# Optimization experiments

Hardware: AMD Instinct MI355X
Metric: run time of the kernel (lower is better)

The kernel has to match this reference:

```python
import jax, jax.numpy as jnp
import numpy as np

B, T, D, H, L, FF, V = 32, 64, 512, 8, 4, 2048, 128
HD = D // H
TEMP = 0.1
SCALE_BASE = 16.0
NEG = -1e9


def setup_inputs() -> dict:
    key = jax.random.key(0)
    cnt = [0]
    def nk():
        cnt[0] += 1
        return jax.random.fold_in(key, cnt[0])
    def rn(shape, s=0.02):
        return jax.random.normal(nk(), shape, dtype=jnp.float32) * s
    inp = {
        "target_tensor": jax.random.randint(nk(), (B, T), 0, V),
        "mol_encoding": jax.random.normal(nk(), (B, D), dtype=jnp.float32),
        "emb": rn((V, D), 1.0),
        "sa_in_w": rn((L, 3 * D, D)), "sa_in_b": jnp.zeros((L, 3 * D), jnp.float32),
        "sa_out_w": rn((L, D, D)), "sa_out_b": jnp.zeros((L, D), jnp.float32),
        "ca_in_w": rn((L, 3 * D, D)), "ca_in_b": jnp.zeros((L, 3 * D), jnp.float32),
        "ca_out_w": rn((L, D, D)), "ca_out_b": jnp.zeros((L, D), jnp.float32),
        "ff_w1": rn((L, FF, D)), "ff_b1": jnp.zeros((L, FF), jnp.float32),
        "ff_w2": rn((L, D, FF)), "ff_b2": jnp.zeros((L, D), jnp.float32),
        "n1_g": jnp.ones((L, D), jnp.float32), "n1_b": jnp.zeros((L, D), jnp.float32),
        "n2_g": jnp.ones((L, D), jnp.float32), "n2_b": jnp.zeros((L, D), jnp.float32),
        "n3_g": jnp.ones((L, D), jnp.float32), "n3_b": jnp.zeros((L, D), jnp.float32),
        "fn_g": jnp.ones((D,), jnp.float32), "fn_b": jnp.zeros((D,), jnp.float32),
        "out_w1": rn((2 * D, D)), "out_b1": jnp.zeros((2 * D,), jnp.float32),
        "out_w2": rn((1024, 2 * D)), "out_b2": jnp.zeros((1024,), jnp.float32),
        "out_w3": rn((V, 1024)), "out_b3": jnp.zeros((V,), jnp.float32),
    }
    return inp


def _ln(x, g, b, eps=1e-5):
    mu = x.mean(-1, keepdims=True)
    var = ((x - mu) ** 2).mean(-1, keepdims=True)
    return (x - mu) * jax.lax.rsqrt(var + eps) * g + b


def _xpos(x):
    # x: [B, T, D]; XPOS rotary with scale_base=16, downscale=False
    t, d = x.shape[1], x.shape[2]
    half = d // 2
    sv = (jnp.arange(0, d, 2, dtype=jnp.float32) + 0.4 * d) / (1.4 * d)      # [half]
    pos = jnp.arange(t, dtype=jnp.float32)
    scale = sv[None, :] ** (pos / SCALE_BASE)[:, None]                       # [t, half]
    inv_freq = 1.0 / (10000.0 ** (jnp.arange(half, dtype=jnp.float32) / half))
    ang = pos[:, None] * inv_freq[None, :]                                   # [t, half]
    sin = jnp.repeat(jnp.sin(ang) * scale, 2, axis=-1)                       # duplicate_interleave
    cos = jnp.repeat(jnp.cos(ang) * scale, 2, axis=-1)
    x1, x2 = x[..., ::2], x[..., 1::2]
    rot = jnp.stack((-x2, x1), axis=-1).reshape(x.shape)                     # rotate_every_two
    return x * cos + rot * sin


def _mha(q_in, k_in, v_in, in_w, in_b, out_w, out_b, mask):
    wq, wk, wv = jnp.split(in_w, 3, axis=0)
    bq, bk, bv = jnp.split(in_b, 3, axis=0)
    Bq, Tq = q_in.shape[0], q_in.shape[1]
    q = (q_in @ wq.T + bq).reshape(Bq, Tq, H, HD)
    k = (k_in @ wk.T + bk).reshape(Bq, -1, H, HD)
    v = (v_in @ wv.T + bv).reshape(Bq, -1, H, HD)
    scores = jnp.einsum('bqhd,bkhd->bhqk', q, k) / np.float32(np.sqrt(HD))
    if mask is not None:
        scores = jnp.where(mask, NEG, scores)
    p = jax.nn.softmax(scores, axis=-1)
    o = jnp.einsum('bhqk,bkhd->bqhd', p, v).reshape(Bq, Tq, D)
    return o @ out_w.T + out_b


def reference(target_tensor, mol_encoding, emb, sa_in_w, sa_in_b, sa_out_w, sa_out_b,
              ca_in_w, ca_in_b, ca_out_w, ca_out_b, ff_w1, ff_b1, ff_w2, ff_b2,
              n1_g, n1_b, n2_g, n2_b, n3_g, n3_b, fn_g, fn_b,
              out_w1, out_b1, out_w2, out_b2, out_w3, out_b3):
    memory = mol_encoding[:, None, :]                      # [B, 1, D]
    causal = jnp.triu(jnp.ones((T, T), bool), 1)
    samp_key = jax.random.key(1)

    def logits_at(pred, t):
        x = _xpos(emb[pred])                               # [B, T, D]
        mask = causal[None, None] | (pred == 0)[:, None, None, :]
        for i in range(L):
            a = _mha(x, x, x, sa_in_w[i], sa_in_b[i], sa_out_w[i], sa_out_b[i], mask)
            x = _ln(x + a, n1_g[i], n1_b[i])
            c = _mha(x, memory, memory, ca_in_w[i], ca_in_b[i], ca_out_w[i], ca_out_b[i], None)
            x = _ln(x + c, n2_g[i], n2_b[i])
            f = jax.nn.silu(x @ ff_w1[i].T + ff_b1[i]) @ ff_w2[i].T + ff_b2[i]
            x = _ln(x + f, n3_g[i], n3_b[i])
        x = _ln(x, fn_g, fn_b)
        h = jnp.take(x, t - 1, axis=1)                     # [B, D]
        h = jax.nn.gelu(h @ out_w1.T + out_b1, approximate=False)
        h = jax.nn.gelu(h @ out_w2.T + out_b2, approximate=False)
        return h @ out_w3.T + out_b3                       # [B, V]

    def step(pred, t):
        logits = logits_at(pred, t)
        lp = jax.nn.log_softmax(logits / TEMP, axis=-1)
        u = jax.random.uniform(jax.random.fold_in(samp_key, t), lp.shape)
        g = -jnp.log(-jnp.log(u + 1e-9) + 1e-9)
        tok = jnp.argmax(lp + g, axis=-1).astype(jnp.int32)
        return pred.at[:, t].set(tok), logits

    pred0 = jnp.zeros((B, T), jnp.int32).at[:, 0].set(1)
    pred, _ = jax.lax.scan(jax.checkpoint(step), pred0, jnp.arange(1, T))
    return pred
```

## Files before the change

kernel.cpp:

```cpp
#include <hip/hip_runtime.h>
#include <stdint.h>
#include <stddef.h>

#define BB 32
#define TT 64
#define DD 512
#define HH 8
#define HDIM 64
#define LL 4
#define FFD 2048
#define VV 128

#define NBLK 256
#define NTHR 512

__host__ __device__ inline uint32_t rotl32(uint32_t v, int n){ return (v << n) | (v >> (32 - n)); }

__host__ __device__ inline void tf2x32(uint32_t k0, uint32_t k1, uint32_t x0, uint32_t x1,
                                       uint32_t* o0, uint32_t* o1){
  uint32_t ks2 = k0 ^ k1 ^ 0x1BD11BDAu;
  x0 += k0; x1 += k1;
  x0 += x1; x1 = rotl32(x1,13); x1 ^= x0;
  x0 += x1; x1 = rotl32(x1,15); x1 ^= x0;
  x0 += x1; x1 = rotl32(x1,26); x1 ^= x0;
  x0 += x1; x1 = rotl32(x1, 6); x1 ^= x0;
  x0 += k1; x1 += ks2 + 1u;
  x0 += x1; x1 = rotl32(x1,17); x1 ^= x0;
  x0 += x1; x1 = rotl32(x1,29); x1 ^= x0;
  x0 += x1; x1 = rotl32(x1,16); x1 ^= x0;
  x0 += x1; x1 = rotl32(x1,24); x1 ^= x0;
  x0 += ks2; x1 += k0 + 2u;
  x0 += x1; x1 = rotl32(x1,13); x1 ^= x0;
  x0 += x1; x1 = rotl32(x1,15); x1 ^= x0;
  x0 += x1; x1 = rotl32(x1,26); x1 ^= x0;
  x0 += x1; x1 = rotl32(x1, 6); x1 ^= x0;
  x0 += k0; x1 += k1 + 3u;
  x0 += x1; x1 = rotl32(x1,17); x1 ^= x0;
  x0 += x1; x1 = rotl32(x1,29); x1 ^= x0;
  x0 += x1; x1 = rotl32(x1,16); x1 ^= x0;
  x0 += x1; x1 = rotl32(x1,24); x1 ^= x0;
  x0 += k1; x1 += ks2 + 4u;
  x0 += x1; x1 = rotl32(x1,13); x1 ^= x0;
  x0 += x1; x1 = rotl32(x1,15); x1 ^= x0;
  x0 += x1; x1 = rotl32(x1,26); x1 ^= x0;
  x0 += x1; x1 = rotl32(x1, 6); x1 ^= x0;
  x0 += ks2; x1 += k0 + 5u;
  *o0 = x0; *o1 = x1;
}

__device__ inline float dot_f4(const float* __restrict__ a, const float* __restrict__ w, int K){
  float acc = 0.f;
  const float4* a4 = (const float4*)a;
  const float4* w4 = (const float4*)w;
  int K4 = K >> 2;
  for (int k = 0; k < K4; ++k){
    float4 av = a4[k], wv = w4[k];
    acc = fmaf(av.x, wv.x, acc);
    acc = fmaf(av.y, wv.y, acc);
    acc = fmaf(av.z, wv.z, acc);
    acc = fmaf(av.w, wv.w, acc);
  }
  return acc;
}

__device__ inline float block_ln(float v, float g, float bb, float* red){
  __syncthreads();
  float s = v;
  #pragma unroll
  for (int off = 32; off; off >>= 1) s += __shfl_xor(s, off);
  if ((threadIdx.x & 63) == 0) red[threadIdx.x >> 6] = s;
  __syncthreads();
  float mu = (red[0]+red[1]+red[2]+red[3]+red[4]+red[5]+red[6]+red[7]) * (1.0f/512.0f);
  float dv = v - mu;
  float sq = dv * dv;
  #pragma unroll
  for (int off = 32; off; off >>= 1) sq += __shfl_xor(sq, off);
  __syncthreads();
  if ((threadIdx.x & 63) == 0) red[threadIdx.x >> 6] = sq;
  __syncthreads();
  float var = (red[0]+red[1]+red[2]+red[3]+red[4]+red[5]+red[6]+red[7]) * (1.0f/512.0f);
  return dv * (1.0f / sqrtf(var + 1e-5f)) * g + bb;
}

__device__ inline float row_reduce(float v, int wid, int j, float* wred){
  #pragma unroll
  for (int off = 32; off; off >>= 1) v += __shfl_xor(v, off);
  if ((threadIdx.x & 63) == 0) wred[wid] = v;
  __syncthreads();
  float r = wred[2*j] + wred[2*j+1];
  __syncthreads();
  return r;
}

__device__ __forceinline__ void gbar(unsigned* bar, int g, int m, unsigned epoch){
  __syncthreads();
  if (threadIdx.x == 0){
    __builtin_amdgcn_fence(__ATOMIC_RELEASE, "agent");
    const int h   = m & 1;
    const int k   = m >> 1;
    const int sub = k >> 3;
    const int gh  = g*2 + h;
    unsigned* subcnt  = bar + gh*64 + sub*16;
    unsigned* halfcnt = bar + 1024 + gh*16;
    unsigned* hflag   = bar + 1280 + gh*16;
    unsigned* peer    = bar + 1280 + (g*2 + (1-h))*16;
    unsigned* hgen    = bar + 1536 + gh*16;
    unsigned old = __hip_atomic_fetch_add(subcnt, 1u, __ATOMIC_RELAXED, __HIP_MEMORY_SCOPE_AGENT);
    if (old == 8u*epoch - 1u){
      unsigned o2 = __hip_atomic_fetch_add(halfcnt, 1u, __ATOMIC_RELAXED, __HIP_MEMORY_SCOPE_AGENT);
      if (o2 == 4u*epoch - 1u){
        __hip_atomic_store(hflag, epoch, __ATOMIC_RELAXED, __HIP_MEMORY_SCOPE_AGENT);
        while (__hip_atomic_load(peer, __ATOMIC_RELAXED, __HIP_MEMORY_SCOPE_AGENT) < epoch)
          __builtin_amdgcn_s_sleep(1);
        __hip_atomic_store(hgen, epoch, __ATOMIC_RELAXED, __HIP_MEMORY_SCOPE_AGENT);
      }
    }
    while (__hip_atomic_load(hgen, __ATOMIC_RELAXED, __HIP_MEMORY_SCOPE_AGENT) < epoch)
      __builtin_amdgcn_s_sleep(1);
    __builtin_amdgcn_fence(__ATOMIC_ACQUIRE, "agent");
  }
  __syncthreads();
}

__global__ void k_tables(float* __restrict__ cosb, float* __restrict__ sinb){
  int tid = blockIdx.x * blockDim.x + threadIdx.x;
  int p = tid >> 8, i = tid & 255;
  float sv = (2.0f * (float)i + 204.8f) / 716.8f;
  float scale = powf(sv, (float)p / 16.0f);
  float invf = 1.0f / powf(10000.0f, (float)i / 256.0f);
  float ang = (float)p * invf;
  cosb[tid] = cosf(ang) * scale;
  sinb[tid] = sinf(ang) * scale;
}

__global__ void k_ca1(const float* __restrict__ mol, const float* __restrict__ w,
                      const float* __restrict__ bias, float* __restrict__ tmp){
  int tid = blockIdx.x * blockDim.x + threadIdx.x;
  int l = tid >> 14; int r = tid & 16383; int b = r >> 9; int d = r & 511;
  const float* wr = w + (size_t)l*3*DD*DD + (size_t)(2*DD + d)*DD;
  tmp[tid] = bias[l*3*DD + 2*DD + d] + dot_f4(mol + (size_t)b*DD, wr, DD);
}

__global__ void k_ca2(const float* __restrict__ tmp, const float* __restrict__ w,
                      const float* __restrict__ bias, float* __restrict__ cac){
  int tid = blockIdx.x * blockDim.x + threadIdx.x;
  int l = tid >> 14; int r = tid & 16383; int b = r >> 9; int d = r & 511;
  const float* wr = w + (size_t)l*DD*DD + (size_t)d*DD;
  cac[tid] = bias[l*DD + d] + dot_f4(tmp + ((size_t)l*BB + b)*DD, wr, DD);
}

__global__ void k_binit(unsigned* __restrict__ bar, int* __restrict__ pred){
  int tid = threadIdx.x;
  bar[tid] = 0u;
  bar[tid + 1024] = 0u;
  pred[tid]        = ((tid & (TT-1)) == 0) ? 1 : 0;
  pred[tid + 1024] = (((tid + 1024) & (TT-1)) == 0) ? 1 : 0;
}

__global__ void k_pack32(const float* __restrict__ in, float* __restrict__ out,
                         int N, int K, int total){
  int tid = blockIdx.x * blockDim.x + threadIdx.x;
  if (tid >= total) return;
  int S = N * K;
  int l = tid / S, r = tid - l*S;
  int k32 = r / (32*N);
  int r2 = r - k32*32*N;
  int n = r2 >> 5, ku = r2 & 31;
  out[tid] = in[(size_t)l*S + (size_t)n*K + k32*32 + ku];
}

#define CELL8(WARR, KOFF)                                                     \
  _Pragma("unroll")                                                           \
  for (int q = 0; q < 8; ++q){                                                \
    float4 w = WARR[q];                                                       \
    const int kk = (KOFF) + q*4;                                              \
    _Pragma("unroll")                                                         \
    for (int r_ = 0; r_ < 8; ++r_){                                           \
      float4 x = *(const float4*)&sxp[r_*512 + kk];                           \
      a[r_]=fmaf(w.x,x.x,a[r_]); a[r_]=fmaf(w.y,x.y,a[r_]);                   \
      a[r_]=fmaf(w.z,x.z,a[r_]); a[r_]=fmaf(w.w,x.w,a[r_]);                   \
    }                                                                         \
  }

struct KParams {
  const float *emb, *sab, *sob, *f1b, *f2b;
  const float *g1,*b1,*g2,*b2,*g3,*b3,*fg,*fb;
  const float *o1b,*o2b,*o3w,*o3b;
  const float *cosb,*sinb,*cac;
  const float *sawP,*sowP,*f1wP,*f2wP,*o1wP,*o2wP;
  float *kc,*vc,*xl,*qb,*at,*ao,*x2,*fo,*h1,*xf,*hh1,*hh2,*ps3;
  int *pred;
  unsigned *bar;
};

__global__ __launch_bounds__(NTHR) void k_persist(KParams P){
  const int bid = blockIdx.x, tid = threadIdx.x;
  const int g = bid & 3;
  const int m = bid >> 2;
  const int wid = tid >> 6, lane = tid & 63;
  __shared__ __align__(16) float smem[17472];
  unsigned epoch = 0;

  for (int t = 1; t < TT; ++t){
    const int pp = t - 1;

    for (int l = 0; l < LL; ++l){
      if (m < 24){
        float* sx   = smem;
        float* part = smem + 4096;
        float* srow = smem + 8192;
        if (l == 0){
          #pragma unroll
          for (int it = 0; it < 2; ++it){
            int j = it*4 + (tid >> 7), d4 = (tid & 127) * 4;
            int rb = g*8 + j;
            int tok = P.pred[rb*TT + pp];
            #pragma unroll
            for (int e = d4; e < d4 + 4; e += 2){
              int i = e >> 1;
              float c = P.cosb[pp*256 + i], s = P.sinb[pp*256 + i];
              float e0 = P.emb[(size_t)tok*DD + e];
              float e1 = P.emb[(size_t)tok*DD + e + 1];
              sx[j*512 + e]     = fmaf(e0, c, -(e1*s));
              sx[j*512 + e + 1] = fmaf(e1, c, e0*s);
            }
          }
        } else {
          if (tid < 8){
            float aa = 0.f, bq = 0.f;
            const float* pr = P.ps3 + (size_t)(g*8 + tid)*64;
            for (int s = 0; s < 32; ++s){ aa += pr[s*2]; bq += pr[s*2+1]; }
            float mu = aa * (1.0f/512.0f);
            float var = bq * (1.0f/512.0f) - mu*mu;
            srow[tid*2]   = mu;
            srow[tid*2+1] = 1.0f / sqrtf(var + 1e-5f);
          }
          __syncthreads();
          #pragma unroll
          for (int it = 0; it < 2; ++it){
            int j = it*4 + (tid >> 7), d4 = (tid & 127) * 4;
            int rb = g*8 + j;
            float mu = srow[j*2], rs = srow[j*2+1];
            float4 xv = *(const float4*)&P.x2[(size_t)rb*DD + d4];
            float4 fv = *(const float4*)&P.fo[(size_t)rb*DD + d4];
            const float* g3r = P.g3 + (size_t)(l-1)*DD;
            const float* b3r = P.b3 + (size_t)(l-1)*DD;
            float yv[4] = {xv.x+fv.x, xv.y+fv.y, xv.z+fv.z, xv.w+fv.w};
            #pragma unroll
            for (int i = 0; i < 4; ++i)
              sx[j*512 + d4 + i] = (yv[i]-mu)*rs*g3r[d4+i] + b3r[d4+i];
          }
        }
        __syncthreads();
        if (m == 0){
          #pragma unroll
          for (int it = 0; it < 2; ++it){
            int j = it*4 + (tid >> 7), d4 = (tid & 127) * 4;
            *(float4*)&P.xl[(size_t)(g*8+j)*DD + d4] = *(float4*)&sx[j*512 + d4];
          }
        }
        const int n0 = m*64;
        const float4* wb0 = (const float4*)P.sawP + ((size_t)l*16 + wid*2)*(1536*8)
                          + (size_t)(n0 + lane)*8;
        const float4* wb1 = wb0 + 1536*8;
        float4 w0[8], w1[8];
        #pragma unroll
        for (int q = 0; q < 8; ++q) w0[q] = wb0[q];
        #pragma unroll
        for (int q = 0; q < 8; ++q) w1[q] = wb1[q];
        float a[8] = {0.f,0.f,0.f,0.f,0.f,0.f,0.f,0.f};
        const float* sxp = sx;
        const int kb = wid*64;
        CELL8(w0, kb);
        CELL8(w1, kb + 32);
        #pragma unroll
        for (int r_ = 0; r_ < 8; ++r_) part[(wid*8 + r_)*64 + lane] = a[r_];
        __syncthreads();
        {
          int jr = tid >> 6, nl = tid & 63;
          int n = n0 + nl, rb2 = g*8 + jr;
          float s = P.sab[l*1536 + n];
          #pragma unroll
          for (int w = 0; w < 8; ++w) s += part[(w*8+jr)*64 + nl];
          if (n < DD){
            P.qb[(size_t)rb2*DD + n] = s;
          } else if (n < 2*DD){
            int h = (n - DD) >> 6, hd = (n - DD) & 63;
            P.kc[((((size_t)l*BB + rb2)*HH + h)*TT + pp)*HDIM + hd] = s;
          } else {
            int h = (n - 2*DD) >> 6, hd = (n - 2*DD) & 63;
            P.vc[((((size_t)l*BB + rb2)*HH + h)*TT + pp)*HDIM + hd] = s;
          }
        }
      }
      gbar(P.bar, g, m, ++epoch);

      {
        int bl = m >> 3, h = m & 7, rb = g*8 + bl;
        float* qs = smem; float* ps = smem + 64;
        if (tid < 64) qs[tid] = P.qb[(size_t)rb*DD + h*HDIM + tid];
        __syncthreads();
        if (tid < 64){
          const float* kb = P.kc + (((size_t)l*BB + rb)*HH + h)*TT*HDIM;
          float s = -INFINITY;
          if (lane <= pp && P.pred[rb*TT + lane] != 0){
            const float* kr = kb + lane*HDIM;
            float acc = 0.f;
            #pragma unroll
            for (int k2 = 0; k2 < HDIM; ++k2) acc = fmaf(qs[k2], kr[k2], acc);
            s = acc * 0.125f;
          }
          float mx = s;
          #pragma unroll
          for (int off = 32; off; off >>= 1) mx = fmaxf(mx, __shfl_xor(mx, off));
          float e = (s == -INFINITY) ? 0.f : expf(s - mx);
          float sum = e;
          #pragma unroll
          for (int off = 32; off; off >>= 1) sum += __shfl_xor(sum, off);
          ps[lane] = e / sum;
          const float* vb = P.vc + (((size_t)l*BB + rb)*HH + h)*TT*HDIM;
          float o = 0.f;
          int jj = 0;
          for (; jj + 8 <= t; jj += 8){
            float vv[8];
            #pragma unroll
            for (int u = 0; u < 8; ++u) vv[u] = vb[(jj+u)*HDIM + lane];
            #pragma unroll
            for (int u = 0; u < 8; ++u) o = fmaf(ps[jj+u], vv[u], o);
          }
          for (; jj <= pp; ++jj) o = fmaf(ps[jj], vb[jj*HDIM + lane], o);
          P.at[(size_t)rb*DD + h*HDIM + lane] = o;
        }
      }
      gbar(P.bar, g, m, ++epoch);

      if (m < 32){
        float* ats  = smem;
        float* part = smem + 4096;
        #pragma unroll
        for (int q = 0; q < 2; ++q){
          int fi = tid + q*512;
          int j = fi >> 7, c4 = fi & 127;
          *(float4*)&ats[j*512 + c4*4] = *(const float4*)&P.at[(size_t)(g*8+j)*DD + c4*4];
        }
        __syncthreads();
        const int n0 = m*16;
        const int jb = lane >> 4, nc = lane & 15;
        const float4* wb0 = (const float4*)P.sowP + ((size_t)l*16 + wid*2)*(512*8)
                          + (size_t)(n0 + nc)*8;
        const float4* wb1 = wb0 + 512*8;
        float4 w0[8], w1[8];
        #pragma unroll
        for (int q = 0; q < 8; ++q) w0[q] = wb0[q];
        #pragma unroll
        for (int q = 0; q < 8; ++q) w1[q] = wb1[q];
        float ac0 = 0.f, ac1 = 0.f;
        const int kb = wid*64;
        #pragma unroll
        for (int q = 0; q < 8; ++q){
          float4 w = w0[q];
          float4 xa = *(const float4*)&ats[jb*512 + kb + q*4];
          float4 xb = *(const float4*)&ats[(jb+4)*512 + kb + q*4];
          ac0=fmaf(w.x,xa.x,ac0); ac0=fmaf(w.y,xa.y,ac0); ac0=fmaf(w.z,xa.z,ac0); ac0=fmaf(w.w,xa.w,ac0);
          ac1=fmaf(w.x,xb.x,ac1); ac1=fmaf(w.y,xb.y,ac1); ac1=fmaf(w.z,xb.z,ac1); ac1=fmaf(w.w,xb.w,ac1);
        }
        #pragma unroll
        for (int q = 0; q < 8; ++q){
          float4 w = w1[q];
          float4 xa = *(const float4*)&ats[jb*512 + kb + 32 + q*4];
          float4 xb = *(const float4*)&ats[(jb+4)*512 + kb + 32 + q*4];
          ac0=fmaf(w.x,xa.x,ac0); ac0=fmaf(w.y,xa.y,ac0); ac0=fmaf(w.z,xa.z,ac0); ac0=fmaf(w.w,xa.w,ac0);
          ac1=fmaf(w.x,xb.x,ac1); ac1=fmaf(w.y,xb.y,ac1); ac1=fmaf(w.z,xb.z,ac1); ac1=fmaf(w.w,xb.w,ac1);
        }
        part[wid*128 + jb*16 + nc]       = ac0;
        part[wid*128 + (jb+4)*16 + nc]   = ac1;
        __syncthreads();
        if (tid < 128){
          int jb2 = tid >> 4, nc2 = tid & 15, n = n0 + nc2;
          float s = P.sob[l*DD + n];
          #pragma unroll
          for (int w = 0; w < 8; ++w) s += part[w*128 + jb2*16 + nc2];
          P.ao[(size_t)(g*8+jb2)*DD + n] = s;
        }
      }
      gbar(P.bar, g, m, ++epoch);

      if (m < 32){
        float* sx2  = smem;
        float* part = smem + 4096;
        float* wred = smem + 8192;
        #pragma unroll
        for (int it = 0; it < 2; ++it){
          int j = tid >> 7, d4 = (tid & 127) * 4;
          int jr = it*4 + j;
          int rb = g*8 + jr;
          float4 xlv = *(const float4*)&P.xl[(size_t)rb*DD + d4];
          float4 aov = *(const float4*)&P.ao[(size_t)rb*DD + d4];
          float y[4] = {xlv.x+aov.x, xlv.y+aov.y, xlv.z+aov.z, xlv.w+aov.w};
          float s = ((y[0]+y[1])+y[2])+y[3];
          float mu = row_reduce(s, wid, j, wred) * (1.0f/512.0f);
          float dv[4], sq = 0.f;
          #pragma unroll
          for (int i = 0; i < 4; ++i){ dv[i] = y[i]-mu; sq += dv[i]*dv[i]; }
          float rs = 1.0f / sqrtf(row_reduce(sq, wid, j, wred) * (1.0f/512.0f) + 1e-5f);
          float z[4];
          #pragma unroll
          for (int i = 0; i < 4; ++i){
            int d = d4 + i;
            z[i] = dv[i]*rs*P.g1[l*DD+d] + P.b1[l*DD+d] + P.cac[((size_t)l*BB + rb)*DD + d];
          }
          float s2 = ((z[0]+z[1])+z[2])+z[3];
          float mu2 = row_reduce(s2, wid, j, wred) * (1.0f/512.0f);
          float dz[4], sq2 = 0.f;
          #pragma unroll
          for (int i = 0; i < 4; ++i){ dz[i] = z[i]-mu2; sq2 += dz[i]*dz[i]; }
          float rs2 = 1.0f / sqrtf(row_reduce(sq2, wid, j, wred) * (1.0f/512.0f) + 1e-5f);
          #pragma unroll
          for (int i = 0; i < 4; ++i){
            int d = d4 + i;
            float x2v = dz[i]*rs2*P.g2[l*DD+d] + P.b2[l*DD+d];
            sx2[jr*512 + d] = x2v;
          }
        }
        __syncthreads();
        if (m == 0){
          #pragma unroll
          for (int it = 0; it < 2; ++it){
            int jr = it*4 + (tid >> 7), d4 = (tid & 127) * 4;
            *(float4*)&P.x2[(size_t)(g*8+jr)*DD + d4] = *(float4*)&sx2[jr*512 + d4];
          }
        }
        const int n0 = m*64;
        const float4* wb0 = (const float4*)P.f1wP + ((size_t)l*16 + wid*2)*(2048*8)
                          + (size_t)(n0 + lane)*8;
        const float4* wb1 = wb0 + 2048*8;
        float4 w0[8], w1[8];
        #pragma unroll
        for (int q = 0; q < 8; ++q) w0[q] = wb0[q];
        #pragma unroll
        for (int q = 0; q < 8; ++q) w1[q] = wb1[q];
        float a[8] = {0.f,0.f,0.f,0.f,0.f,0.f,0.f,0.f};
        const float* sxp = sx2;
        const int kb = wid*64;
        CELL8(w0, kb);
        CELL8(w1, kb + 32);
        #pragma unroll
        for (int r_ = 0; r_ < 8; ++r_) part[(wid*8 + r_)*64 + lane] = a[r_];
        __syncthreads();
        {
          int jr = tid >> 6, nl = tid & 63;
          int n = n0 + nl;
          float v = P.f1b[l*FFD + n];
          #pragma unroll
          for (int w = 0; w < 8; ++w) v += part[(w*8+jr)*64 + nl];
          P.h1[(size_t)(g*8+jr)*FFD + n] = v / (1.0f + expf(-v));
        }
      }
      gbar(P.bar, g, m, ++epoch);

      if (m < 32){
        float* sh1  = smem;
        float* part = smem + 16384;
        #pragma unroll
        for (int q = 0; q < 8; ++q){
          int fi = tid + q*512;
          int j = fi >> 9, c4 = fi & 511;
          *(float4*)&sh1[j*2048 + c4*4] = *(const float4*)&P.h1[(size_t)(g*8+j)*FFD + c4*4];
        }
        __syncthreads();
        const int n0 = m*16;
        const int jb = lane >> 4, nc = lane & 15;
        const float4* base = (const float4*)P.f2wP + ((size_t)l*64 + wid*8)*(512*8)
                           + (size_t)(n0 + nc)*8;
        float ac0 = 0.f, ac1 = 0.f;
        #pragma unroll
        for (int cc = 0; cc < 4; ++cc){
          const float4* b0 = base + (size_t)(cc*2)*(512*8);
          const float4* b1 = b0 + 512*8;
          float4 w0[8], w1[8];
          #pragma unroll
          for (int q = 0; q < 8; ++q) w0[q] = b0[q];
          #pragma unroll
          for (int q = 0; q < 8; ++q) w1[q] = b1[q];
          const int kb = wid*256 + cc*64;
          #pragma unroll
          for (int q = 0; q < 8; ++q){
            float4 w = w0[q];
            float4 xa = *(const float4*)&sh1[jb*2048 + kb + q*4];
            float4 xb = *(const float4*)&sh1[(jb+4)*2048 + kb + q*4];
            ac0=fmaf(w.x,xa.x,ac0); ac0=fmaf(w.y,xa.y,ac0); ac0=fmaf(w.z,xa.z,ac0); ac0=fmaf(w.w,xa.w,ac0);
            ac1=fmaf(w.x,xb.x,ac1); ac1=fmaf(w.y,xb.y,ac1); ac1=fmaf(w.z,xb.z,ac1); ac1=fmaf(w.w,xb.w,ac1);
          }
          #pragma unroll
          for (int q = 0; q < 8; ++q){
            float4 w = w1[q];
            float4 xa = *(const float4*)&sh1[jb*2048 + kb + 32 + q*4];
            float4 xb = *(const float4*)&sh1[(jb+4)*2048 + kb + 32 + q*4];
            ac0=fmaf(w.x,xa.x,ac0); ac0=fmaf(w.y,xa.y,ac0); ac0=fmaf(w.z,xa.z,ac0); ac0=fmaf(w.w,xa.w,ac0);
            ac1=fmaf(w.x,xb.x,ac1); ac1=fmaf(w.y,xb.y,ac1); ac1=fmaf(w.z,xb.z,ac1); ac1=fmaf(w.w,xb.w,ac1);
          }
        }
        part[wid*128 + jb*16 + nc]     = ac0;
        part[wid*128 + (jb+4)*16 + nc] = ac1;
        __syncthreads();
        if (tid < 128){
          int jb2 = tid >> 4, nc2 = tid & 15, n = n0 + nc2;
          int rb2 = g*8 + jb2;
          float val = P.f2b[l*DD + n];
          #pragma unroll
          for (int w = 0; w < 8; ++w) val += part[w*128 + jb2*16 + nc2];
          P.fo[(size_t)rb2*DD + n] = val;
          float y = P.x2[(size_t)rb2*DD + n] + val;
          float s1 = y, sq = y*y;
          #pragma unroll
          for (int off = 1; off < 16; off <<= 1){
            s1 += __shfl_xor(s1, off);
            sq += __shfl_xor(sq, off);
          }
          if (nc2 == 0){
            P.ps3[(size_t)(rb2*32 + m)*2]     = s1;
            P.ps3[(size_t)(rb2*32 + m)*2 + 1] = sq;
          }
        }
      }
      gbar(P.bar, g, m, ++epoch);
    }

    if (m < 8){
      int rb = g*8 + m, d = tid;
      float y = P.x2[(size_t)rb*DD + d] + P.fo[(size_t)rb*DD + d];
      float xv = block_ln(y, P.g3[3*DD + d], P.b3[3*DD + d], smem);
      float o  = block_ln(xv, P.fg[d], P.fb[d], smem);
      P.xf[(size_t)rb*DD + d] = o;
    }
    gbar(P.bar, g, m, ++epoch);

    if (m < 32){
      float* sxf  = smem;
      float* part = smem + 4096;
      #pragma unroll
      for (int q = 0; q < 2; ++q){
        int fi = tid + q*512;
        int j = fi >> 7, c4 = fi & 127;
        *(float4*)&sxf[j*512 + c4*4] = *(const float4*)&P.xf[(size_t)(g*8+j)*DD + c4*4];
      }
      __syncthreads();
      const int n0 = m*32;
      const int jh = lane >> 5, nc = lane & 31;
      const float4* wb0 = (const float4*)P.o1wP + (size_t)(wid*2)*(1024*8)
                        + (size_t)(n0 + nc)*8;
      const float4* wb1 = wb0 + 1024*8;
      float4 w0[8], w1[8];
      #pragma unroll
      for (int q = 0; q < 8; ++q) w0[q] = wb0[q];
      #pragma unroll
      for (int q = 0; q < 8; ++q) w1[q] = wb1[q];
      float ac[4] = {0.f,0.f,0.f,0.f};
      const int kb = wid*64;
      #pragma unroll
      for (int q = 0; q < 8; ++q){
        float4 w = w0[q];
        #pragma unroll
        for (int ai = 0; ai < 4; ++ai){
          float4 x = *(const float4*)&sxf[(jh+2*ai)*512 + kb + q*4];
          ac[ai]=fmaf(w.x,x.x,ac[ai]); ac[ai]=fmaf(w.y,x.y,ac[ai]);
          ac[ai]=fmaf(w.z,x.z,ac[ai]); ac[ai]=fmaf(w.w,x.w,ac[ai]);
        }
      }
      #pragma unroll
      for (int q = 0; q < 8; ++q){
        float4 w = w1[q];
        #pragma unroll
        for (int ai = 0; ai < 4; ++ai){
          float4 x = *(const float4*)&sxf[(jh+2*ai)*512 + kb + 32 + q*4];
          ac[ai]=fmaf(w.x,x.x,ac[ai]); ac[ai]=fmaf(w.y,x.y,ac[ai]);
          ac[ai]=fmaf(w.z,x.z,ac[ai]); ac[ai]=fmaf(w.w,x.w,ac[ai]);
        }
      }
      #pragma unroll
      for (int ai = 0; ai < 4; ++ai) part[(wid*8 + (jh+2*ai))*32 + nc] = ac[ai];
      __syncthreads();
      if (tid < 256){
        int row = tid >> 5, nc2 = tid & 31, n = n0 + nc2;
        float aa = P.o1b[n];
        #pragma unroll
        for (int w = 0; w < 8; ++w) aa += part[(w*8+row)*32 + nc2];
        P.hh1[(size_t)(g*8+row)*1024 + n] = 0.5f * aa * (1.0f + erff(aa / 1.41421356237309504880f));
      }
    }
    gbar(P.bar, g, m, ++epoch);

    if (m < 32){
      float* sh   = smem;
      float* part = smem + 8192;
      #pragma unroll
      for (int q = 0; q < 4; ++q){
        int fi = tid + q*512;
        int j = fi >> 8, c4 = fi & 255;
        *(float4*)&sh[j*1024 + c4*4] = *(const float4*)&P.hh1[(size_t)(g*8+j)*1024 + c4*4];
      }
      __syncthreads();
      const int n0 = m*32;
      const int jh = lane >> 5, nc = lane & 31;
      const float4* base = (const float4*)P.o2wP + (size_t)(wid*4)*(1024*8)
                         + (size_t)(n0 + nc)*8;
      float ac[4] = {0.f,0.f,0.f,0.f};
      #pragma unroll
      for (int cc = 0; cc < 2; ++cc){
        const float4* b0 = base + (size_t)(cc*2)*(1024*8);
        const float4* b1 = b0 + 1024*8;
        float4 w0[8], w1[8];
        #pragma unroll
        for (int q = 0; q < 8; ++q) w0[q] = b0[q];
        #pragma unroll
        for (int q = 0; q < 8; ++q) w1[q] = b1[q];
        const int kb = wid*128 + cc*64;
        #pragma unroll
        for (int q = 0; q < 8; ++q){
          float4 w = w0[q];
          #pragma unroll
          for (int ai = 0; ai < 4; ++ai){
            float4 x = *(const float4*)&sh[(jh+2*ai)*1024 + kb + q*4];
            ac[ai]=fmaf(w.x,x.x,ac[ai]); ac[ai]=fmaf(w.y,x.y,ac[ai]);
            ac[ai]=fmaf(w.z,x.z,ac[ai]); ac[ai]=fmaf(w.w,x.w,ac[ai]);
          }
        }
        #pragma unroll
        for (int q = 0; q < 8; ++q){
          float4 w = w1[q];
          #pragma unroll
          for (int ai = 0; ai < 4; ++ai){
            float4 x = *(const float4*)&sh[(jh+2*ai)*1024 + kb + 32 + q*4];
            ac[ai]=fmaf(w.x,x.x,ac[ai]); ac[ai]=fmaf(w.y,x.y,ac[ai]);
            ac[ai]=fmaf(w.z,x.z,ac[ai]); ac[ai]=fmaf(w.w,x.w,ac[ai]);
          }
        }
      }
      #pragma unroll
      for (int ai = 0; ai < 4; ++ai) part[(wid*8 + (jh+2*ai))*32 + nc] = ac[ai];
      __syncthreads();
      if (tid < 256){
        int row = tid >> 5, nc2 = tid & 31, n = n0 + nc2;
        float aa = P.o2b[n];
        #pragma unroll
        for (int w = 0; w < 8; ++w) aa += part[(w*8+row)*32 + nc2];
        P.hh2[(size_t)(g*8+row)*1024 + n] = 0.5f * aa * (1.0f + erff(aa / 1.41421356237309504880f));
      }
    }
    gbar(P.bar, g, m, ++epoch);

    if (m < 8){
      int rb = g*8 + m, v = tid;
      float* hrow = smem;
      float* red  = smem + 1024;
      int*   redi = (int*)(smem + 1032);
      for (int k = tid; k < 1024; k += NTHR) hrow[k] = P.hh2[(size_t)rb*1024 + k];
      __syncthreads();
      float sv = 0.f;
      if (tid < 128){
        float acc = P.o3b[v] + dot_f4(hrow, P.o3w + (size_t)v*1024, 1024);
        sv = acc / 0.1f;
      }
      float mx = (tid < 128) ? sv : -INFINITY;
      #pragma unroll
      for (int off = 32; off; off >>= 1) mx = fmaxf(mx, __shfl_xor(mx, off));
      __syncthreads();
      if (tid < 128 && (tid & 63) == 0) red[tid >> 6] = mx;
      __syncthreads();
      mx = fmaxf(red[0], red[1]);
      float e = (tid < 128) ? expf(sv - mx) : 0.f;
      float sum = e;
      #pragma unroll
      for (int off = 32; off; off >>= 1) sum += __shfl_xor(sum, off);
      __syncthreads();
      if (tid < 128 && (tid & 63) == 0) red[tid >> 6] = sum;
      __syncthreads();
      sum = red[0] + red[1];
      float bv = -INFINITY; int bi = 0x7fffffff;
      if (tid < 128){
        float lp = (sv - mx) - logf(sum);
        uint32_t kk0, kk1, o0, o1;
        tf2x32(0u, 1u, 0u, (uint32_t)t, &kk0, &kk1);
        tf2x32(kk0, kk1, 0u, (uint32_t)(rb*VV + v), &o0, &o1);
        uint32_t bits = o0 ^ o1;
        float u = __uint_as_float((bits >> 9) | 0x3F800000u) - 1.0f;
        float gg = -logf(-logf(u + 1e-9f) + 1e-9f);
        bv = lp + gg; bi = v;
      }
      #pragma unroll
      for (int off = 32; off; off >>= 1){
        float ov = __shfl_xor(bv, off);
        int   oi = __shfl_xor(bi, off);
        if (ov > bv || (ov == bv && oi < bi)){ bv = ov; bi = oi; }
      }
      __syncthreads();
      if (tid < 128 && (tid & 63) == 0){ red[tid >> 6] = bv; redi[tid >> 6] = bi; }
      __syncthreads();
      if (tid == 0){
        float v0 = red[0], v1 = red[1]; int i0 = redi[0], i1 = redi[1];
        P.pred[rb*TT + t] = (v1 > v0 || (v1 == v0 && i1 < i0)) ? i1 : i0;
      }
    }
    gbar(P.bar, g, m, ++epoch);
  }
}

extern "C" void kernel_launch(void* const* d_in, const int* in_sizes, int n_in,
                              void* d_out, int out_size, void* d_ws, size_t ws_size,
                              hipStream_t stream){
  (void)in_sizes; (void)n_in; (void)out_size; (void)ws_size;
  const float* mol      = (const float*)d_in[1];
  const float* sa_in_w  = (const float*)d_in[3];
  const float* sa_out_w = (const float*)d_in[5];
  const float* ca_in_w  = (const float*)d_in[7];
  const float* ca_in_b  = (const float*)d_in[8];
  const float* ca_out_w = (const float*)d_in[9];
  const float* ca_out_b = (const float*)d_in[10];
  const float* ff_w1    = (const float*)d_in[11];
  const float* ff_w2    = (const float*)d_in[13];
  const float* out_w1   = (const float*)d_in[23];
  const float* out_w2   = (const float*)d_in[25];

  KParams P;
  P.emb = (const float*)d_in[2];
  P.sab = (const float*)d_in[4];
  P.sob = (const float*)d_in[6];
  P.f1b = (const float*)d_in[12];
  P.f2b = (const float*)d_in[14];
  P.g1  = (const float*)d_in[15];
  P.b1  = (const float*)d_in[16];
  P.g2  = (const float*)d_in[17];
  P.b2  = (const float*)d_in[18];
  P.g3  = (const float*)d_in[19];
  P.b3  = (const float*)d_in[20];
  P.fg  = (const float*)d_in[21];
  P.fb  = (const float*)d_in[22];
  P.o1b = (const float*)d_in[24];
  P.o2b = (const float*)d_in[26];
  P.o3w = (const float*)d_in[27];
  P.o3b = (const float*)d_in[28];

  unsigned* bar = (unsigned*)d_ws;
  float* ws = (float*)d_ws + 2048;
  float* cosb   = ws;
  float* sinb   = cosb + 16384;
  float* ca_tmp = sinb + 16384;
  float* cac    = ca_tmp + 65536;
  float* kc     = cac + 65536;
  float* vc     = kc + 4194304;
  float* xl     = vc + 4194304;
  float* qb     = xl + 16384;
  float* at     = qb + 16384;
  float* ao     = at + 16384;
  float* x2     = ao + 16384;
  float* fo     = x2 + 16384;
  float* h1     = fo + 16384;
  float* xf     = h1 + 65536;
  float* hh1    = xf + 16384;
  float* hh2    = hh1 + 32768;
  float* ps3    = hh2 + 32768;
  float* sawP   = ps3 + 2048;
  float* sowP   = sawP + 3145728;
  float* f1wP   = sowP + 1048576;
  float* f2wP   = f1wP + 4194304;
  float* o1wP   = f2wP + 4194304;
  float* o2wP   = o1wP + 524288;

  P.cosb = cosb; P.sinb = sinb; P.cac = cac;
  P.kc = kc; P.vc = vc; P.xl = xl; P.qb = qb; P.at = at; P.ao = ao;
  P.x2 = x2; P.fo = fo; P.h1 = h1; P.xf = xf; P.hh1 = hh1; P.hh2 = hh2;
  P.ps3 = ps3;
  P.sawP = sawP; P.sowP = sowP; P.f1wP = f1wP; P.f2wP = f2wP;
  P.o1wP = o1wP; P.o2wP = o2wP;
  P.pred = (int*)d_out;
  P.bar = bar;

  k_binit<<<1, 1024, 0, stream>>>(bar, P.pred);
  k_tables<<<64, 256, 0, stream>>>(cosb, sinb);
  k_ca1<<<256, 256, 0, stream>>>(mol, ca_in_w, ca_in_b, ca_tmp);
  k_ca2<<<256, 256, 0, stream>>>(ca_tmp, ca_out_w, ca_out_b, cac);

  {
    int t1 = 4*1536*512;  k_pack32<<<(t1+255)/256, 256, 0, stream>>>(sa_in_w,  sawP, 1536, 512,  t1);
    int t2 = 4*512*512;   k_pack32<<<(t2+255)/256, 256, 0, stream>>>(sa_out_w, sowP,  512, 512,  t2);
    int t3 = 4*2048*512;  k_pack32<<<(t3+255)/256, 256, 0, stream>>>(ff_w1,    f1wP, 2048, 512,  t3);
    int t4 = 4*512*2048;  k_pack32<<<(t4+255)/256, 256, 0, stream>>>(ff_w2,    f2wP,  512, 2048, t4);
    int t5 = 1024*512;    k_pack32<<<(t5+255)/256, 256, 0, stream>>>(out_w1,   o1wP, 1024, 512,  t5);
    int t6 = 1024*1024;   k_pack32<<<(t6+255)/256, 256, 0, stream>>>(out_w2,   o2wP, 1024, 1024, t6);
  }

  k_persist<<<NBLK, NTHR, 0, stream>>>(P);
}
```

Baseline: 24.77 ms.

## Spread every GEMV phase across all 64 blocks per group with narrower column tiles

Each persistent-kernel GEMV phase (QKV projection, attention output, FFN up and down, and both output-head layers) previously used only 24 or 32 of the 64 blocks per batch group. The column tile per block is halved so all 64 blocks take part, with each lane computing fewer rows and the LayerNorm partial-sum buffer doubled to hold 64 partials. The aim is to finish each phase sooner between grid barriers by using more CUs for the weight streaming. In exchange, per-block arithmetic intensity drops, more blocks stream weights, and reduction threads are halved.

Measured after the change: 24.10 ms. 2.7% less time.

```diff
diff --git a/kernel.cpp b/kernel.cpp
--- a/kernel.cpp
+++ b/kernel.cpp
@@ -169,17 +169,19 @@
   out[tid] = in[(size_t)l*S + (size_t)n*K + k32*32 + ku];
 }
 
-#define CELL8(WARR, KOFF)                                                     \
+#define CELL4(WARR, KOFF)                                                     \
   _Pragma("unroll")                                                           \
   for (int q = 0; q < 8; ++q){                                                \
     float4 w = WARR[q];                                                       \
     const int kk = (KOFF) + q*4;                                              \
-    _Pragma("unroll")                                                         \
-    for (int r_ = 0; r_ < 8; ++r_){                                           \
-      float4 x = *(const float4*)&sxp[r_*512 + kk];                           \
-      a[r_]=fmaf(w.x,x.x,a[r_]); a[r_]=fmaf(w.y,x.y,a[r_]);                   \
-      a[r_]=fmaf(w.z,x.z,a[r_]); a[r_]=fmaf(w.w,x.w,a[r_]);                   \
-    }                                                                         \
+    float4 xa = *(const float4*)&sxp[0*512 + kk];                             \
+    float4 xb = *(const float4*)&sxp[1*512 + kk];                             \
+    float4 xc = *(const float4*)&sxp[2*512 + kk];                             \
+    float4 xd = *(const float4*)&sxp[3*512 + kk];                             \
+    a0=fmaf(w.x,xa.x,a0); a0=fmaf(w.y,xa.y,a0); a0=fmaf(w.z,xa.z,a0); a0=fmaf(w.w,xa.w,a0); \
+    a1=fmaf(w.x,xb.x,a1); a1=fmaf(w.y,xb.y,a1); a1=fmaf(w.z,xb.z,a1); a1=fmaf(w.w,xb.w,a1); \
+    a2=fmaf(w.x,xc.x,a2); a2=fmaf(w.y,xc.y,a2); a2=fmaf(w.z,xc.z,a2); a2=fmaf(w.w,xc.w,a2); \
+    a3=fmaf(w.x,xd.x,a3); a3=fmaf(w.y,xd.y,a3); a3=fmaf(w.z,xd.z,a3); a3=fmaf(w.w,xd.w,a3); \
   }
 
 struct KParams {
@@ -205,10 +207,10 @@
     const int pp = t - 1;
 
     for (int l = 0; l < LL; ++l){
-      if (m < 24){
+      if (m < 48){
         float* sx   = smem;
         float* part = smem + 4096;
-        float* srow = smem + 8192;
+        float* srow = smem + 6144;
         if (l == 0){
           #pragma unroll
           for (int it = 0; it < 2; ++it){
@@ -228,8 +230,11 @@
         } else {
           if (tid < 8){
             float aa = 0.f, bq = 0.f;
-            const float* pr = P.ps3 + (size_t)(g*8 + tid)*64;
-            for (int s = 0; s < 32; ++s){ aa += pr[s*2]; bq += pr[s*2+1]; }
+            const float* pr = P.ps3 + (size_t)(g*8 + tid)*128;
+            for (int s = 0; s < 32; ++s){
+              aa += (pr[4*s]     + pr[4*s + 2]);
+              bq += (pr[4*s + 1] + pr[4*s + 3]);
+            }
             float mu = aa * (1.0f/512.0f);
             float var = bq * (1.0f/512.0f) - mu*mu;
             srow[tid*2]   = mu;
@@ -259,29 +264,32 @@
             *(float4*)&P.xl[(size_t)(g*8+j)*DD + d4] = *(float4*)&sx[j*512 + d4];
           }
         }
-        const int n0 = m*64;
+        const int n0 = m*32;
+        const int c = lane & 31, rh = lane >> 5;
         const float4* wb0 = (const float4*)P.sawP + ((size_t)l*16 + wid*2)*(1536*8)
-                          + (size_t)(n0 + lane)*8;
+                          + (size_t)(n0 + c)*8;
         const float4* wb1 = wb0 + 1536*8;
         float4 w0[8], w1[8];
         #pragma unroll
         for (int q = 0; q < 8; ++q) w0[q] = wb0[q];
         #pragma unroll
         for (int q = 0; q < 8; ++q) w1[q] = wb1[q];
-        float a[8] = {0.f,0.f,0.f,0.f,0.f,0.f,0.f,0.f};
-        const float* sxp = sx;
+        float a0=0.f,a1=0.f,a2=0.f,a3=0.f;
+        const float* sxp = sx + rh*4*512;
         const int kb = wid*64;
-        CELL8(w0, kb);
-        CELL8(w1, kb + 32);
-        #pragma unroll
-        for (int r_ = 0; r_ < 8; ++r_) part[(wid*8 + r_)*64 + lane] = a[r_];
-        __syncthreads();
-        {
-          int jr = tid >> 6, nl = tid & 63;
+        CELL4(w0, kb);
+        CELL4(w1, kb + 32);
+        part[(wid*8 + rh*4 + 0)*32 + c] = a0;
+        part[(wid*8 + rh*4 + 1)*32 + c] = a1;
+        part[(wid*8 + rh*4 + 2)*32 + c] = a2;
+        part[(wid*8 + rh*4 + 3)*32 + c] = a3;
+        __syncthreads();
+        if (tid < 256){
+          int jr = tid >> 5, nl = tid & 31;
           int n = n0 + nl, rb2 = g*8 + jr;
           float s = P.sab[l*1536 + n];
           #pragma unroll
-          for (int w = 0; w < 8; ++w) s += part[(w*8+jr)*64 + nl];
+          for (int w = 0; w < 8; ++w) s += part[(w*8+jr)*32 + nl];
           if (n < DD){
             P.qb[(size_t)rb2*DD + n] = s;
           } else if (n < 2*DD){
@@ -334,7 +342,7 @@
       }
       gbar(P.bar, g, m, ++epoch);
 
-      if (m < 32){
+      {
         float* ats  = smem;
         float* part = smem + 4096;
         #pragma unroll
@@ -344,8 +352,8 @@
           *(float4*)&ats[j*512 + c4*4] = *(const float4*)&P.at[(size_t)(g*8+j)*DD + c4*4];
         }
         __syncthreads();
-        const int n0 = m*16;
-        const int jb = lane >> 4, nc = lane & 15;
+        const int n0 = m*8;
+        const int jb = lane >> 3, nc = lane & 7;
         const float4* wb0 = (const float4*)P.sowP + ((size_t)l*16 + wid*2)*(512*8)
                           + (size_t)(n0 + nc)*8;
         const float4* wb1 = wb0 + 512*8;
@@ -354,41 +362,36 @@
         for (int q = 0; q < 8; ++q) w0[q] = wb0[q];
         #pragma unroll
         for (int q = 0; q < 8; ++q) w1[q] = wb1[q];
-        float ac0 = 0.f, ac1 = 0.f;
+        float acc = 0.f;
         const int kb = wid*64;
         #pragma unroll
         for (int q = 0; q < 8; ++q){
           float4 w = w0[q];
           float4 xa = *(const float4*)&ats[jb*512 + kb + q*4];
-          float4 xb = *(const float4*)&ats[(jb+4)*512 + kb + q*4];
-          ac0=fmaf(w.x,xa.x,ac0); ac0=fmaf(w.y,xa.y,ac0); ac0=fmaf(w.z,xa.z,ac0); ac0=fmaf(w.w,xa.w,ac0);
-          ac1=fmaf(w.x,xb.x,ac1); ac1=fmaf(w.y,xb.y,ac1); ac1=fmaf(w.z,xb.z,ac1); ac1=fmaf(w.w,xb.w,ac1);
+          acc=fmaf(w.x,xa.x,acc); acc=fmaf(w.y,xa.y,acc); acc=fmaf(w.z,xa.z,acc); acc=fmaf(w.w,xa.w,acc);
         }
         #pragma unroll
         for (int q = 0; q < 8; ++q){
           float4 w = w1[q];
           float4 xa = *(const float4*)&ats[jb*512 + kb + 32 + q*4];
-          float4 xb = *(const float4*)&ats[(jb+4)*512 + kb + 32 + q*4];
-          ac0=fmaf(w.x,xa.x,ac0); ac0=fmaf(w.y,xa.y,ac0); ac0=fmaf(w.z,xa.z,ac0); ac0=fmaf(w.w,xa.w,ac0);
-          ac1=fmaf(w.x,xb.x,ac1); ac1=fmaf(w.y,xb.y,ac1); ac1=fmaf(w.z,xb.z,ac1); ac1=fmaf(w.w,xb.w,ac1);
-        }
-        part[wid*128 + jb*16 + nc]       = ac0;
-        part[wid*128 + (jb+4)*16 + nc]   = ac1;
-        __syncthreads();
-        if (tid < 128){
-          int jb2 = tid >> 4, nc2 = tid & 15, n = n0 + nc2;
+          acc=fmaf(w.x,xa.x,acc); acc=fmaf(w.y,xa.y,acc); acc=fmaf(w.z,xa.z,acc); acc=fmaf(w.w,xa.w,acc);
+        }
+        part[wid*64 + jb*8 + nc] = acc;
+        __syncthreads();
+        if (tid < 64){
+          int jb2 = tid >> 3, nc2 = tid & 7, n = n0 + nc2;
           float s = P.sob[l*DD + n];
           #pragma unroll
-          for (int w = 0; w < 8; ++w) s += part[w*128 + jb2*16 + nc2];
+          for (int w = 0; w < 8; ++w) s += part[w*64 + jb2*8 + nc2];
           P.ao[(size_t)(g*8+jb2)*DD + n] = s;
         }
       }
       gbar(P.bar, g, m, ++epoch);
 
-      if (m < 32){
+      {
         float* sx2  = smem;
         float* part = smem + 4096;
-        float* wred = smem + 8192;
+        float* wred = smem + 6144;
         #pragma unroll
         for (int it = 0; it < 2; ++it){
           int j = tid >> 7, d4 = (tid & 127) * 4;
@@ -418,8 +421,7 @@
           #pragma unroll
           for (int i = 0; i < 4; ++i){
             int d = d4 + i;
-            float x2v = dz[i]*rs2*P.g2[l*DD+d] + P.b2[l*DD+d];
-            sx2[jr*512 + d] = x2v;
+            sx2[jr*512 + d] = dz[i]*rs2*P.g2[l*DD+d] + P.b2[l*DD+d];
           }
         }
         __syncthreads();
@@ -430,35 +432,38 @@
             *(float4*)&P.x2[(size_t)(g*8+jr)*DD + d4] = *(float4*)&sx2[jr*512 + d4];
           }
         }
-        const int n0 = m*64;
+        const int n0 = m*32;
+        const int c = lane & 31, rh = lane >> 5;
         const float4* wb0 = (const float4*)P.f1wP + ((size_t)l*16 + wid*2)*(2048*8)
-                          + (size_t)(n0 + lane)*8;
+                          + (size_t)(n0 + c)*8;
         const float4* wb1 = wb0 + 2048*8;
         float4 w0[8], w1[8];
         #pragma unroll
         for (int q = 0; q < 8; ++q) w0[q] = wb0[q];
         #pragma unroll
         for (int q = 0; q < 8; ++q) w1[q] = wb1[q];
-        float a[8] = {0.f,0.f,0.f,0.f,0.f,0.f,0.f,0.f};
-        const float* sxp = sx2;
+        float a0=0.f,a1=0.f,a2=0.f,a3=0.f;
+        const float* sxp = sx2 + rh*4*512;
         const int kb = wid*64;
-        CELL8(w0, kb);
-        CELL8(w1, kb + 32);
-        #pragma unroll
-        for (int r_ = 0; r_ < 8; ++r_) part[(wid*8 + r_)*64 + lane] = a[r_];
-        __syncthreads();
-        {
-          int jr = tid >> 6, nl = tid & 63;
+        CELL4(w0, kb);
+        CELL4(w1, kb + 32);
+        part[(wid*8 + rh*4 + 0)*32 + c] = a0;
+        part[(wid*8 + rh*4 + 1)*32 + c] = a1;
+        part[(wid*8 + rh*4 + 2)*32 + c] = a2;
+        part[(wid*8 + rh*4 + 3)*32 + c] = a3;
+        __syncthreads();
+        if (tid < 256){
+          int jr = tid >> 5, nl = tid & 31;
           int n = n0 + nl;
           float v = P.f1b[l*FFD + n];
           #pragma unroll
-          for (int w = 0; w < 8; ++w) v += part[(w*8+jr)*64 + nl];
+          for (int w = 0; w < 8; ++w) v += part[(w*8+jr)*32 + nl];
           P.h1[(size_t)(g*8+jr)*FFD + n] = v / (1.0f + expf(-v));
         }
       }
       gbar(P.bar, g, m, ++epoch);
 
-      if (m < 32){
+      {
         float* sh1  = smem;
         float* part = smem + 16384;
         #pragma unroll
@@ -468,11 +473,11 @@
           *(float4*)&sh1[j*2048 + c4*4] = *(const float4*)&P.h1[(size_t)(g*8+j)*FFD + c4*4];
         }
         __syncthreads();
-        const int n0 = m*16;
-        const int jb = lane >> 4, nc = lane & 15;
+        const int n0 = m*8;
+        const int jb = lane >> 3, nc = lane & 7;
         const float4* base = (const float4*)P.f2wP + ((size_t)l*64 + wid*8)*(512*8)
                            + (size_t)(n0 + nc)*8;
-        float ac0 = 0.f, ac1 = 0.f;
+        float acc = 0.f;
         #pragma unroll
         for (int cc = 0; cc < 4; ++cc){
           const float4* b0 = base + (size_t)(cc*2)*(512*8);
@@ -487,39 +492,34 @@
           for (int q = 0; q < 8; ++q){
             float4 w = w0[q];
             float4 xa = *(const float4*)&sh1[jb*2048 + kb + q*4];
-            float4 xb = *(const float4*)&sh1[(jb+4)*2048 + kb + q*4];
-            ac0=fmaf(w.x,xa.x,ac0); ac0=fmaf(w.y,xa.y,ac0); ac0=fmaf(w.z,xa.z,ac0); ac0=fmaf(w.w,xa.w,ac0);
-            ac1=fmaf(w.x,xb.x,ac1); ac1=fmaf(w.y,xb.y,ac1); ac1=fmaf(w.z,xb.z,ac1); ac1=fmaf(w.w,xb.w,ac1);
+            acc=fmaf(w.x,xa.x,acc); acc=fmaf(w.y,xa.y,acc); acc=fmaf(w.z,xa.z,acc); acc=fmaf(w.w,xa.w,acc);
           }
           #pragma unroll
           for (int q = 0; q < 8; ++q){
             float4 w = w1[q];
             float4 xa = *(const float4*)&sh1[jb*2048 + kb + 32 + q*4];
-            float4 xb = *(const float4*)&sh1[(jb+4)*2048 + kb + 32 + q*4];
-            ac0=fmaf(w.x,xa.x,ac0); ac0=fmaf(w.y,xa.y,ac0); ac0=fmaf(w.z,xa.z,ac0); ac0=fmaf(w.w,xa.w,ac0);
-            ac1=fmaf(w.x,xb.x,ac1); ac1=fmaf(w.y,xb.y,ac1); ac1=fmaf(w.z,xb.z,ac1); ac1=fmaf(w.w,xb.w,ac1);
-          }
-        }
-        part[wid*128 + jb*16 + nc]     = ac0;
-        part[wid*128 + (jb+4)*16 + nc] = ac1;
-        __syncthreads();
-        if (tid < 128){
-          int jb2 = tid >> 4, nc2 = tid & 15, n = n0 + nc2;
+            acc=fmaf(w.x,xa.x,acc); acc=fmaf(w.y,xa.y,acc); acc=fmaf(w.z,xa.z,acc); acc=fmaf(w.w,xa.w,acc);
+          }
+        }
+        part[wid*64 + jb*8 + nc] = acc;
+        __syncthreads();
+        if (tid < 64){
+          int jb2 = tid >> 3, nc2 = tid & 7, n = n0 + nc2;
           int rb2 = g*8 + jb2;
           float val = P.f2b[l*DD + n];
           #pragma unroll
-          for (int w = 0; w < 8; ++w) val += part[w*128 + jb2*16 + nc2];
+          for (int w = 0; w < 8; ++w) val += part[w*64 + jb2*8 + nc2];
           P.fo[(size_t)rb2*DD + n] = val;
           float y = P.x2[(size_t)rb2*DD + n] + val;
           float s1 = y, sq = y*y;
           #pragma unroll
-          for (int off = 1; off < 16; off <<= 1){
+          for (int off = 1; off < 8; off <<= 1){
             s1 += __shfl_xor(s1, off);
             sq += __shfl_xor(sq, off);
           }
           if (nc2 == 0){
-            P.ps3[(size_t)(rb2*32 + m)*2]     = s1;
-            P.ps3[(size_t)(rb2*32 + m)*2 + 1] = sq;
+            P.ps3[(size_t)(rb2*64 + m)*2]     = s1;
+            P.ps3[(size_t)(rb2*64 + m)*2 + 1] = sq;
           }
         }
       }
@@ -535,7 +535,7 @@
     }
     gbar(P.bar, g, m, ++epoch);
 
-    if (m < 32){
+    {
       float* sxf  = smem;
       float* part = smem + 4096;
       #pragma unroll
@@ -545,8 +545,8 @@
         *(float4*)&sxf[j*512 + c4*4] = *(const float4*)&P.xf[(size_t)(g*8+j)*DD + c4*4];
       }
       __syncthreads();
-      const int n0 = m*32;
-      const int jh = lane >> 5, nc = lane & 31;
+      const int n0 = m*16;
+      const int p = lane >> 4, nc = lane & 15;
       const float4* wb0 = (const float4*)P.o1wP + (size_t)(wid*2)*(1024*8)
                         + (size_t)(n0 + nc)*8;
       const float4* wb1 = wb0 + 1024*8;
@@ -555,42 +555,38 @@
       for (int q = 0; q < 8; ++q) w0[q] = wb0[q];
       #pragma unroll
       for (int q = 0; q < 8; ++q) w1[q] = wb1[q];
-      float ac[4] = {0.f,0.f,0.f,0.f};
+      float ac0 = 0.f, ac1 = 0.f;
       const int kb = wid*64;
       #pragma unroll
       for (int q = 0; q < 8; ++q){
         float4 w = w0[q];
-        #pragma unroll
-        for (int ai = 0; ai < 4; ++ai){
-          float4 x = *(const float4*)&sxf[(jh+2*ai)*512 + kb + q*4];
-          ac[ai]=fmaf(w.x,x.x,ac[ai]); ac[ai]=fmaf(w.y,x.y,ac[ai]);
-          ac[ai]=fmaf(w.z,x.z,ac[ai]); ac[ai]=fmaf(w.w,x.w,ac[ai]);
-        }
+        float4 xa = *(const float4*)&sxf[p*512 + kb + q*4];
+        float4 xb = *(const float4*)&sxf[(p+4)*512 + kb + q*4];
+        ac0=fmaf(w.x,xa.x,ac0); ac0=fmaf(w.y,xa.y,ac0); ac0=fmaf(w.z,xa.z,ac0); ac0=fmaf(w.w,xa.w,ac0);
+        ac1=fmaf(w.x,xb.x,ac1); ac1=fmaf(w.y,xb.y,ac1); ac1=fmaf(w.z,xb.z,ac1); ac1=fmaf(w.w,xb.w,ac1);
       }
       #pragma unroll
       for (int q = 0; q < 8; ++q){
         float4 w = w1[q];
-        #pragma unroll
-        for (int ai = 0; ai < 4; ++ai){
-          float4 x = *(const float4*)&sxf[(jh+2*ai)*512 + kb + 32 + q*4];
-          ac[ai]=fmaf(w.x,x.x,ac[ai]); ac[ai]=fmaf(w.y,x.y,ac[ai]);
-          ac[ai]=fmaf(w.z,x.z,ac[ai]); ac[ai]=fmaf(w.w,x.w,ac[ai]);
-        }
-      }
-      #pragma unroll
-      for (int ai = 0; ai < 4; ++ai) part[(wid*8 + (jh+2*ai))*32 + nc] = ac[ai];
-      __syncthreads();
-      if (tid < 256){
-        int row = tid >> 5, nc2 = tid & 31, n = n0 + nc2;
+        float4 xa = *(const float4*)&sxf[p*512 + kb + 32 + q*4];
+        float4 xb = *(const float4*)&sxf[(p+4)*512 + kb + 32 + q*4];
+        ac0=fmaf(w.x,xa.x,ac0); ac0=fmaf(w.y,xa.y,ac0); ac0=fmaf(w.z,xa.z,ac0); ac0=fmaf(w.w,xa.w,ac0);
+        ac1=fmaf(w.x,xb.x,ac1); ac1=fmaf(w.y,xb.y,ac1); ac1=fmaf(w.z,xb.z,ac1); ac1=fmaf(w.w,xb.w,ac1);
+      }
+      part[(wid*8 + p)*16 + nc]     = ac0;
+      part[(wid*8 + p + 4)*16 + nc] = ac1;
+      __syncthreads();
+      if (tid < 128){
+        int row = tid >> 4, nc2 = tid & 15, n = n0 + nc2;
         float aa = P.o1b[n];
         #pragma unroll
-        for (int w = 0; w < 8; ++w) aa += part[(w*8+row)*32 + nc2];
+        for (int w = 0; w < 8; ++w) aa += part[(w*8+row)*16 + nc2];
         P.hh1[(size_t)(g*8+row)*1024 + n] = 0.5f * aa * (1.0f + erff(aa / 1.41421356237309504880f));
       }
     }
     gbar(P.bar, g, m, ++epoch);
 
-    if (m < 32){
+    {
       float* sh   = smem;
       float* part = smem + 8192;
       #pragma unroll
@@ -600,11 +596,11 @@
         *(float4*)&sh[j*1024 + c4*4] = *(const float4*)&P.hh1[(size_t)(g*8+j)*1024 + c4*4];
       }
       __syncthreads();
-      const int n0 = m*32;
-      const int jh = lane >> 5, nc = lane & 31;
+      const int n0 = m*16;
+      const int p = lane >> 4, nc = lane & 15;
       const float4* base = (const float4*)P.o2wP + (size_t)(wid*4)*(1024*8)
                          + (size_t)(n0 + nc)*8;
-      float ac[4] = {0.f,0.f,0.f,0.f};
+      float ac0 = 0.f, ac1 = 0.f;
       #pragma unroll
       for (int cc = 0; cc < 2; ++cc){
         const float4* b0 = base + (size_t)(cc*2)*(1024*8);
@@ -618,32 +614,28 @@
         #pragma unroll
         for (int q = 0; q < 8; ++q){
           float4 w = w0[q];
-          #pragma unroll
-          for (int ai = 0; ai < 4; ++ai){
-            float4 x = *(const float4*)&sh[(jh+2*ai)*1024 + kb + q*4];
-            ac[ai]=fmaf(w.x,x.x,ac[ai]); ac[ai]=fmaf(w.y,x.y,ac[ai]);
-            ac[ai]=fmaf(w.z,x.z,ac[ai]); ac[ai]=fmaf(w.w,x.w,ac[ai]);
-          }
+          float4 xa = *(const float4*)&sh[p*1024 + kb + q*4];
+          float4 xb = *(const float4*)&sh[(p+4)*1024 + kb + q*4];
+          ac0=fmaf(w.x,xa.x,ac0); ac0=fmaf(w.y,xa.y,ac0); ac0=fmaf(w.z,xa.z,ac0); ac0=fmaf(w.w,xa.w,ac0);
+          ac1=fmaf(w.x,xb.x,ac1); ac1=fmaf(w.y,xb.y,ac1); ac1=fmaf(w.z,xb.z,ac1); ac1=fmaf(w.w,xb.w,ac1);
         }
         #pragma unroll
         for (int q = 0; q < 8; ++q){
           float4 w = w1[q];
-          #pragma unroll
-          for (int ai = 0; ai < 4; ++ai){
-            float4 x = *(const float4*)&sh[(jh+2*ai)*1024 + kb + 32 + q*4];
-            ac[ai]=fmaf(w.x,x.x,ac[ai]); ac[ai]=fmaf(w.y,x.y,ac[ai]);
-            ac[ai]=fmaf(w.z,x.z,ac[ai]); ac[ai]=fmaf(w.w,x.w,ac[ai]);
-          }
-        }
-      }
-      #pragma unroll
-      for (int ai = 0; ai < 4; ++ai) part[(wid*8 + (jh+2*ai))*32 + nc] = ac[ai];
-      __syncthreads();
-      if (tid < 256){
-        int row = tid >> 5, nc2 = tid & 31, n = n0 + nc2;
+          float4 xa = *(const float4*)&sh[p*1024 + kb + 32 + q*4];
+          float4 xb = *(const float4*)&sh[(p+4)*1024 + kb + 32 + q*4];
+          ac0=fmaf(w.x,xa.x,ac0); ac0=fmaf(w.y,xa.y,ac0); ac0=fmaf(w.z,xa.z,ac0); ac0=fmaf(w.w,xa.w,ac0);
+          ac1=fmaf(w.x,xb.x,ac1); ac1=fmaf(w.y,xb.y,ac1); ac1=fmaf(w.z,xb.z,ac1); ac1=fmaf(w.w,xb.w,ac1);
+        }
+      }
+      part[(wid*8 + p)*16 + nc]     = ac0;
+      part[(wid*8 + p + 4)*16 + nc] = ac1;
+      __syncthreads();
+      if (tid < 128){
+        int row = tid >> 4, nc2 = tid & 15, n = n0 + nc2;
         float aa = P.o2b[n];
         #pragma unroll
-        for (int w = 0; w < 8; ++w) aa += part[(w*8+row)*32 + nc2];
+        for (int w = 0; w < 8; ++w) aa += part[(w*8+row)*16 + nc2];
         P.hh2[(size_t)(g*8+row)*1024 + n] = 0.5f * aa * (1.0f + erff(aa / 1.41421356237309504880f));
       }
     }
@@ -759,7 +751,7 @@
   float* hh1    = xf + 16384;
   float* hh2    = hh1 + 32768;
   float* ps3    = hh2 + 32768;
-  float* sawP   = ps3 + 2048;
+  float* sawP   = ps3 + 4096;
   float* sowP   = sawP + 3145728;
   float* f1wP   = sowP + 1048576;
   float* f2wP   = f1wP + 4194304;
```
